# Optimization experiments

Hardware: AMD Instinct MI355X
Metric: run time of the kernel (lower is better)

Reference implementation:

```python
import jax, jax.numpy as jnp
import numpy as np

B, S, H, E = 64, 512, 768, 8
HID = 256

def setup_inputs() -> dict:
    key = jax.random.key(0)
    ks = jax.random.split(key, 20)
    seq = jax.random.normal(ks[0], (B, S, H), dtype=jnp.float32)
    starts = jax.random.randint(ks[1], (B, E), 0, S - 16)
    spans = jax.random.randint(ks[2], (B, E), 0, 12)
    ends = jnp.minimum(starts + spans, S - 1)
    w = lambda k, shp: (jax.random.normal(k, shp, dtype=jnp.float32) * 0.02)
    return {
        "sequence_output": seq,
        "entity_start_positions": starts,
        "entity_end_positions": ends,
        "mW1": w(ks[3], (3 * H, HID)), "mb1": jnp.zeros((HID,), jnp.float32),
        "mW2": w(ks[4], (HID, 3)),     "mb2": jnp.zeros((3,), jnp.float32),
        "pW1": w(ks[5], (3 * H, HID)), "pb1": jnp.zeros((HID,), jnp.float32),
        "pW2": w(ks[6], (HID, 6)),     "pb2": jnp.zeros((6,), jnp.float32),
        "aW1": w(ks[7], (3 * H, HID)), "ab1": jnp.zeros((HID,), jnp.float32),
        "aW2": w(ks[8], (HID, 12)),    "ab2": jnp.zeros((12,), jnp.float32),
        "iW1": w(ks[9], (3 * H, HID)), "ib1": jnp.zeros((HID,), jnp.float32),
        "iW2": w(ks[10], (HID, 4)),    "ib2": jnp.zeros((4,), jnp.float32),
    }

def _mlp(x, W1, b1, W2, b2):
    return jax.nn.relu(x @ W1 + b1) @ W2 + b2  # dropout is inference no-op

def reference(sequence_output, entity_start_positions, entity_end_positions,
              mW1, mb1, mW2, mb2, pW1, pb1, pW2, pb2,
              aW1, ab1, aW2, ab2, iW1, ib1, iW2, ib2):
    Bs, Ss, Hs = sequence_output.shape
    dt = sequence_output.dtype
    # prefix sums: P[b, t] = sum of tokens [0, t)
    P = jnp.concatenate([jnp.zeros((Bs, 1, Hs), dt), jnp.cumsum(sequence_output, axis=1)], axis=1)  # [B,S+1,H]
    s = entity_start_positions  # [B,E]
    e = entity_end_positions    # [B,E]
    bidx = jnp.arange(Bs)[:, None]
    Ps = P[bidx, s]          # [B,E,H] sum of tokens [0, start)
    Pe1 = P[bidx, e + 1]     # [B,E,H] sum of tokens [0, end+1)
    Ptot = P[:, Ss][:, None, :]  # [B,1,H]
    left_n = s.astype(dt)[..., None]
    span_n = (e - s + 1).astype(dt)[..., None]
    right_cnt = (Ss - (e + 1))
    right_n = right_cnt.astype(dt)[..., None]
    left = jnp.where(s[..., None] > 0, Ps / jnp.maximum(left_n, 1.0), 0.0)
    span = (Pe1 - Ps) / span_n
    right = jnp.where(right_cnt[..., None] > 0, (Ptot - Pe1) / jnp.maximum(right_n, 1.0), 0.0)
    emb = jnp.concatenate([left, span, right], axis=-1).reshape(-1, 3 * Hs)  # [N, 3H]
    main_logits = _mlp(emb, mW1, mb1, mW2, mb2)            # [N,3]
    main_probs = jax.nn.softmax(main_logits, axis=-1)
    pred = jnp.argmax(main_probs, axis=-1)                 # [N]
    lp = jax.nn.sigmoid(_mlp(emb, pW1, pb1, pW2, pb2))     # [N,6]
    la = jax.nn.sigmoid(_mlp(emb, aW1, ab1, aW2, ab2))     # [N,12]
    li = jax.nn.sigmoid(_mlp(emb, iW1, ib1, iW2, ib2))     # [N,4]
    fp = jnp.pad(lp, ((0, 0), (0, 16)))
    fa = jnp.pad(la, ((0, 0), (6, 4)))
    fi = jnp.pad(li, ((0, 0), (18, 0)))
    r = pred[:, None]
    fine = jnp.where(r == 0, fp, jnp.where(r == 1, fa, fi))  # [N,22]
    return main_logits, main_probs, fine
```

## Files before the change

### kernel.cpp

```cpp
#include <hip/hip_runtime.h>

#define HH   768
#define SS   512
#define BB   64
#define NE   512
#define K3   2304
#define HID  256
#define NCH  16
#define CRW  32
#define NCOL 1280

typedef __attribute__((ext_vector_type(4))) float  f32x4;
typedef _Float16 f16;
typedef __attribute__((ext_vector_type(8))) _Float16 f16x8;
typedef __attribute__((ext_vector_type(4))) _Float16 f16x4;

__global__ __launch_bounds__(192) void k_scan(
    const float* __restrict__ seq, const int* __restrict__ starts,
    const int* __restrict__ ends, const float* __restrict__ pW1,
    const float* __restrict__ aW1, const float* __restrict__ iW1,
    const float* __restrict__ mW1,
    float* __restrict__ chunkSum, float* __restrict__ cap,
    f16* __restrict__ wT)
{
  __shared__ float Ls[48 * 65];
  const int bx = blockIdx.x;
  const int t  = threadIdx.x;

  if (bx < BB * NCH) {
    const int b = bx >> 4, c = bx & 15;
    int ev[16];
#pragma unroll
    for (int j = 0; j < 8; j++) {
      ev[j]     = starts[b * 8 + j];
      ev[8 + j] = ends[b * 8 + j] + 1;
    }
    unsigned rowhit = 0;
#pragma unroll
    for (int j = 0; j < 16; j++) {
      const int d = ev[j] - c * CRW;
      if ((unsigned)d < 32u) rowhit |= (1u << d);
    }
    const float* base = seq + ((size_t)(b * SS + c * CRW)) * HH + t * 4;
    f32x4 run = {0.f, 0.f, 0.f, 0.f};
#pragma unroll 8
    for (int r = 0; r < CRW; r++) {
      const int s = c * CRW + r;
      if (rowhit & (1u << r)) {
#pragma unroll
        for (int j = 0; j < 16; j++) {
          if (ev[j] == s)
            *(f32x4*)(cap + ((size_t)(b * 16 + j)) * HH + t * 4) = run;
        }
      }
      f32x4 v = *(const f32x4*)(base + (size_t)r * HH);
      run += v;
    }
    *(f32x4*)(chunkSum + ((size_t)(b * 16 + c)) * HH + t * 4) = run;
  } else {
    const int bi   = bx - BB * NCH;
    const int slot = bi / 192;
    const int r    = bi % 192;
    const int kt = r >> 2, nt = r & 3;
    const int k0 = kt * 48, n0 = nt * 64;
    const float* W = (slot == 0) ? pW1 : ((slot == 1) ? aW1 :
                     ((slot == 2) ? iW1 : mW1));
#pragma unroll
    for (int p = 0; p < 4; p++) {
      const int row = (t >> 4) + p * 12;
      const int col = (t & 15) * 4;
      f32x4 v = *(const f32x4*)(W + (size_t)(k0 + row) * HID + n0 + col);
      Ls[row * 65 + col + 0] = v.x;
      Ls[row * 65 + col + 1] = v.y;
      Ls[row * 65 + col + 2] = v.z;
      Ls[row * 65 + col + 3] = v.w;
    }
    __syncthreads();
    const int n = t / 3, u = t % 3;
    if (slot < 3) {
#pragma unroll
      for (int j = 0; j < 2; j++) {
        const int kb = u * 16 + j * 8;
        f16x8 pk;
#pragma unroll
        for (int i = 0; i < 8; i++) pk[i] = (f16)Ls[(kb + i) * 65 + n];
        *(f16x8*)(wT + (size_t)(slot * 256 + n0 + n) * K3 + k0 + kb) = pk;
      }
    } else {
#pragma unroll
      for (int j = 0; j < 2; j++) {
        const int kb = u * 16 + j * 8;
        f16x8 ph, pl;
#pragma unroll
        for (int i = 0; i < 8; i++) {
          const float x = Ls[(kb + i) * 65 + n];
          const f16 h = (f16)x;
          ph[i] = h;
          pl[i] = (f16)(x - (float)h);
        }
        *(f16x8*)(wT + (size_t)(768  + n0 + n) * K3 + k0 + kb) = ph;
        *(f16x8*)(wT + (size_t)(1024 + n0 + n) * K3 + k0 + kb) = pl;
      }
    }
  }
}

__global__ __launch_bounds__(192) void k_emb(
    const float* __restrict__ chunkSum, const float* __restrict__ cap,
    const int* __restrict__ starts, const int* __restrict__ ends,
    f16* __restrict__ embH)
{
  const int bx = blockIdx.x;
  const int t  = threadIdx.x;
  const int b = bx >> 3, e = bx & 7;
  const int s  = starts[b * 8 + e];
  const int en = ends[b * 8 + e];
  const int cs = s >> 5, ce = (en + 1) >> 5;

  const float* csb = chunkSum + (size_t)(b * 16) * HH + t * 4;
  f32x4 acc = {0.f, 0.f, 0.f, 0.f};
  f32x4 baseS = {0.f, 0.f, 0.f, 0.f}, baseE = {0.f, 0.f, 0.f, 0.f};
#pragma unroll
  for (int c = 0; c < 16; c++) {
    if (c == cs) baseS = acc;
    if (c == ce) baseE = acc;
    acc += *(const f32x4*)(csb + (size_t)c * HH);
  }
  f32x4 capS = *(const f32x4*)(cap + (size_t)(b * 16 + e) * HH + t * 4);
  f32x4 capE = *(const f32x4*)(cap + (size_t)(b * 16 + 8 + e) * HH + t * 4);
  f32x4 Ps = baseS + capS;
  f32x4 Pe = baseE + capE;
  f32x4 Pt = acc;

  f32x4 zero = {0.f, 0.f, 0.f, 0.f};
  f32x4 left = zero;
  if (s > 0) left = Ps * (1.0f / (float)s);
  f32x4 span = (Pe - Ps) * (1.0f / (float)(en - s + 1));
  const int rc = SS - (en + 1);
  f32x4 right = zero;
  if (rc > 0) right = (Pt - Pe) * (1.0f / (float)rc);

  f16* ob = embH + (size_t)bx * K3 + t * 4;
  f16x4 p0, p1, p2;
#pragma unroll
  for (int i = 0; i < 4; i++) {
    p0[i] = (f16)left[i];
    p1[i] = (f16)span[i];
    p2[i] = (f16)right[i];
  }
  *(f16x4*)(ob)        = p0;
  *(f16x4*)(ob + 768)  = p1;
  *(f16x4*)(ob + 1536) = p2;
}

__global__ __launch_bounds__(256) void k_gemm(
    const f16* __restrict__ embH, const f16* __restrict__ wT,
    float* __restrict__ Hall)
{
  __shared__ __align__(16) char smem[55296];
  const int bx0 = blockIdx.x;
  const int bx  = (bx0 & 7) * 40 + (bx0 >> 3);
  const int t  = threadIdx.x;
  const int mt = bx & 15, nt = bx >> 4;
  const int m0 = mt * 32, nG0 = nt * 64;

  const int l = t & 63, w = t >> 6;
  const int w2 = w & 1;
  const int kw = w >> 1;
  const int klane = l >> 4;
  const int lr = l & 15;
  f32x4 acc[2][2] = {};

  const int am = t >> 3, ako = (t & 7) * 8;
  const f16* gA = embH + (size_t)(m0 + am) * K3 + ako;
  const int aoff = am * 72 + ako;
  const int bn0 = t >> 3,        bko0 = (t & 7) * 8;
  const int bn1 = (t + 256) >> 3, bko1 = (t & 7) * 8;
  const f16* gB0 = wT + (size_t)(nG0 + bn0) * K3 + bko0;
  const f16* gB1 = wT + (size_t)(nG0 + bn1) * K3 + bko1;
  const int boff0 = bn0 * 72 + bko0, boff1 = bn1 * 72 + bko1;

  f16x8 pA, pB0, pB1, qA, qB0, qB1;

#define LOADSET(S, KT) { const int kn_ = (KT) * 64;                       \
    S##A  = *(const f16x8*)(gA  + kn_);                                   \
    S##B0 = *(const f16x8*)(gB0 + kn_);                                   \
    S##B1 = *(const f16x8*)(gB1 + kn_); }

#define WRITESET(S, BUF) { f16* An_ = (f16*)(smem + (BUF) * 13824);       \
    f16* Bn_ = An_ + 2304;                                                \
    *(f16x8*)(An_ + aoff)  = S##A;                                        \
    *(f16x8*)(Bn_ + boff0) = S##B0;                                       \
    *(f16x8*)(Bn_ + boff1) = S##B1; }

#define COMPUTE(BUF) { f16* Ac_ = (f16*)(smem + (BUF) * 13824);           \
    f16* Bc_ = Ac_ + 2304;                                                \
    const int koff_ = kw * 32 + klane * 8;                                \
    f16x8 aW[2], bE[2];                                                   \
    _Pragma("unroll")                                                     \
    for (int f = 0; f < 2; f++) {                                         \
      aW[f] = *(const f16x8*)(Bc_ + (w2 * 32 + f * 16 + lr) * 72 + koff_);\
      bE[f] = *(const f16x8*)(Ac_ + (f * 16 + lr) * 72 + koff_);          \
    }                                                                     \
    _Pragma("unroll")                                                     \
    for (int fn = 0; fn < 2; fn++)                                        \
      _Pragma("unroll")                                                   \
      for (int fm = 0; fm < 2; fm++)                                      \
        acc[fn][fm] = __builtin_amdgcn_mfma_f32_16x16x32_f16(             \
            aW[fn], bE[fm], acc[fn][fm], 0, 0, 0); }

  LOADSET(p, 0);
  LOADSET(q, 1);
  WRITESET(p, 0);
  WRITESET(q, 1);
  __syncthreads();

  for (int kt = 0; kt < 36; kt += 2) {
    const bool pre = (kt < 34);
    if (pre) { LOADSET(p, kt + 2); LOADSET(q, kt + 3); }
    COMPUTE(kt & 3);
    COMPUTE((kt + 1) & 3);
    if (pre) { WRITESET(p, (kt + 2) & 3); WRITESET(q, (kt + 3) & 3); }
    __syncthreads();
  }
#undef LOADSET
#undef WRITESET
#undef COMPUTE

  float* Lt = (float*)smem;
  if (kw == 1) {
#pragma unroll
    for (int fn = 0; fn < 2; fn++)
#pragma unroll
      for (int fm = 0; fm < 2; fm++) {
        const int nl = w2 * 32 + fn * 16 + klane * 4;
        const int ml = fm * 16 + lr;
        *(f32x4*)(Lt + ml * 68 + nl) = acc[fn][fm];
      }
  }
  __syncthreads();
  if (kw == 0) {
#pragma unroll
    for (int fn = 0; fn < 2; fn++)
#pragma unroll
      for (int fm = 0; fm < 2; fm++) {
        const int nl = w2 * 32 + fn * 16 + klane * 4;
        const int ml = fm * 16 + lr;
        f32x4* pd = (f32x4*)(Lt + ml * 68 + nl);
        *pd = *pd + acc[fn][fm];
      }
  }
  __syncthreads();
  const int row = t >> 3, cb = (t & 7) * 8;
  float* dst = Hall + (size_t)(m0 + row) * NCOL + nG0 + cb;
  const float* src = Lt + row * 68 + cb;
  *(f32x4*)(dst)     = *(const f32x4*)(src);
  *(f32x4*)(dst + 4) = *(const f32x4*)(src + 4);
}

__global__ __launch_bounds__(256) void k_head(
    const float* __restrict__ Hall,
    const float* __restrict__ mb1, const float* __restrict__ mW2, const float* __restrict__ mb2,
    const float* __restrict__ pb1, const float* __restrict__ pW2, const float* __restrict__ pb2,
    const float* __restrict__ ab1, const float* __restrict__ aW2, const float* __restrict__ ab2,
    const float* __restrict__ ib1, const float* __restrict__ iW2, const float* __restrict__ ib2,
    float* __restrict__ out)
{
  __shared__ float red[4][15];
  const int m = blockIdx.x;
  const int t = threadIdx.x;
  const int l = t & 63, wi = t >> 6;
  const int n = t;
  const float* hrow = Hall + (size_t)m * NCOL;

  float h = hrow[768 + n] + hrow[1024 + n] + mb1[n];
  h = h > 0.f ? h : 0.f;
  float am0 = h * mW2[n * 3 + 0];
  float am1 = h * mW2[n * 3 + 1];
  float am2 = h * mW2[n * 3 + 2];

  float hp = hrow[n] + pb1[n];
  hp = hp > 0.f ? hp : 0.f;
  float ha = hrow[256 + n] + ab1[n];
  ha = ha > 0.f ? ha : 0.f;
  float hv = hrow[512 + n] + ib1[n];
  hv = hv > 0.f ? hv : 0.f;

#pragma unroll
  for (int d = 1; d < 64; d <<= 1) {
    am0 += __shfl_xor(am0, d);
    am1 += __shfl_xor(am1, d);
    am2 += __shfl_xor(am2, d);
  }
  if (l == 0) { red[wi][0] = am0; red[wi][1] = am1; red[wi][2] = am2; }
  __syncthreads();

  const float l0 = red[0][0] + red[1][0] + red[2][0] + red[3][0] + mb2[0];
  const float l1 = red[0][1] + red[1][1] + red[2][1] + red[3][1] + mb2[1];
  const float l2 = red[0][2] + red[1][2] + red[2][2] + red[3][2] + mb2[2];
  int pred = 0;
  {
    float pbv = l0;
    if (l1 > pbv) { pbv = l1; pred = 1; }
    if (l2 > pbv) { pbv = l2; pred = 2; }
  }

  if (pred == 0) {
    float ap[6];
#pragma unroll
    for (int o = 0; o < 6; o++) ap[o] = hp * pW2[n * 6 + o];
#pragma unroll
    for (int d = 1; d < 64; d <<= 1)
#pragma unroll
      for (int o = 0; o < 6; o++) ap[o] += __shfl_xor(ap[o], d);
    if (l == 0)
#pragma unroll
      for (int o = 0; o < 6; o++) red[wi][3 + o] = ap[o];
  } else if (pred == 1) {
    float aa[12];
#pragma unroll
    for (int o = 0; o < 12; o++) aa[o] = ha * aW2[n * 12 + o];
#pragma unroll
    for (int d = 1; d < 64; d <<= 1)
#pragma unroll
      for (int o = 0; o < 12; o++) aa[o] += __shfl_xor(aa[o], d);
    if (l == 0)
#pragma unroll
      for (int o = 0; o < 12; o++) red[wi][3 + o] = aa[o];
  } else {
    float ai[4];
#pragma unroll
    for (int o = 0; o < 4; o++) ai[o] = hv * iW2[n * 4 + o];
#pragma unroll
    for (int d = 1; d < 64; d <<= 1)
#pragma unroll
      for (int o = 0; o < 4; o++) ai[o] += __shfl_xor(ai[o], d);
    if (l == 0)
#pragma unroll
      for (int o = 0; o < 4; o++) red[wi][3 + o] = ai[o];
  }
  __syncthreads();

  if (t == 0) {
    const float mx = fmaxf(l0, fmaxf(l1, l2));
    const float e0 = expf(l0 - mx), e1 = expf(l1 - mx), e2 = expf(l2 - mx);
    const float inv = 1.0f / (e0 + e1 + e2);
    const float p0 = e0 * inv, p1 = e1 * inv, p2 = e2 * inv;

    out[m * 3 + 0] = l0;
    out[m * 3 + 1] = l1;
    out[m * 3 + 2] = l2;
    out[1536 + m * 3 + 0] = p0;
    out[1536 + m * 3 + 1] = p1;
    out[1536 + m * 3 + 2] = p2;

    float f[22];
#pragma unroll
    for (int j = 0; j < 22; j++) f[j] = 0.f;
    if (pred == 0) {
#pragma unroll
      for (int j = 0; j < 6; j++) {
        const float v = red[0][3 + j] + red[1][3 + j] + red[2][3 + j] + red[3][3 + j];
        f[j] = 1.0f / (1.0f + expf(-(v + pb2[j])));
      }
    } else if (pred == 1) {
#pragma unroll
      for (int j = 0; j < 12; j++) {
        const float v = red[0][3 + j] + red[1][3 + j] + red[2][3 + j] + red[3][3 + j];
        f[6 + j] = 1.0f / (1.0f + expf(-(v + ab2[j])));
      }
    } else {
#pragma unroll
      for (int j = 0; j < 4; j++) {
        const float v = red[0][3 + j] + red[1][3 + j] + red[2][3 + j] + red[3][3 + j];
        f[18 + j] = 1.0f / (1.0f + expf(-(v + ib2[j])));
      }
    }
#pragma unroll
    for (int j = 0; j < 22; j++) out[3072 + m * 22 + j] = f[j];
  }
}

extern "C" void kernel_launch(void* const* d_in, const int* in_sizes, int n_in,
                              void* d_out, int out_size, void* d_ws, size_t ws_size,
                              hipStream_t stream)
{
  const float* seq    = (const float*)d_in[0];
  const int*   starts = (const int*)d_in[1];
  const int*   ends   = (const int*)d_in[2];
  const float* mW1 = (const float*)d_in[3];
  const float* mb1 = (const float*)d_in[4];
  const float* mW2 = (const float*)d_in[5];
  const float* mb2 = (const float*)d_in[6];
  const float* pW1 = (const float*)d_in[7];
  const float* pb1 = (const float*)d_in[8];
  const float* pW2 = (const float*)d_in[9];
  const float* pb2 = (const float*)d_in[10];
  const float* aW1 = (const float*)d_in[11];
  const float* ab1 = (const float*)d_in[12];
  const float* aW2 = (const float*)d_in[13];
  const float* ab2 = (const float*)d_in[14];
  const float* iW1 = (const float*)d_in[15];
  const float* ib1 = (const float*)d_in[16];
  const float* iW2 = (const float*)d_in[17];
  const float* ib2 = (const float*)d_in[18];

  char* ws = (char*)d_ws;
  float* chunkSum = (float*)(ws);
  float* cap      = (float*)(ws + 3145728);
  f16*   embH     = (f16*)(ws + 6291456);
  f16*   wT       = (f16*)(ws + 8650752);
  float* Hall     = (float*)(ws + 14548992);

  k_scan<<<dim3(1792), dim3(192), 0, stream>>>(seq, starts, ends, pW1, aW1, iW1, mW1,
                                               chunkSum, cap, wT);
  k_emb<<<dim3(512), dim3(192), 0, stream>>>(chunkSum, cap, starts, ends, embH);
  k_gemm<<<dim3(320), dim3(256), 0, stream>>>(embH, wT, Hall);
  k_head<<<dim3(512), dim3(256), 0, stream>>>(Hall,
                                              mb1, mW2, mb2, pb1, pW2, pb2,
                                              ab1, aW2, ab2, ib1, iW2, ib2,
                                              (float*)d_out);
}
```

Before: 50.36 us.

## Load GEMM weight fragments directly from global into registers, bypassing LDS

The GEMM kernel now reads each wave's B (weight) MFMA fragments straight from global memory into registers instead of staging them through shared memory. Only the A (embedding) tile is still staged through LDS, now double-buffered with two barriers per k-step pair. This shrinks LDS from about 54KB to 9KB, which may allow more resident blocks. In exchange, the global reads for B are less coalesced (each lane reads 16 bytes from a different row), and the extra barrier per iteration adds synchronization.

```diff
diff --git a/kernel.cpp b/kernel.cpp
--- a/kernel.cpp
+++ b/kernel.cpp
@@ -157,7 +157,7 @@
     const f16* __restrict__ embH, const f16* __restrict__ wT,
     float* __restrict__ Hall)
 {
-  __shared__ __align__(16) char smem[55296];
+  __shared__ __align__(16) char smem[9216];
   const int bx0 = blockIdx.x;
   const int bx  = (bx0 & 7) * 40 + (bx0 >> 3);
   const int t  = threadIdx.x;
@@ -174,57 +174,48 @@
   const int am = t >> 3, ako = (t & 7) * 8;
   const f16* gA = embH + (size_t)(m0 + am) * K3 + ako;
   const int aoff = am * 72 + ako;
-  const int bn0 = t >> 3,        bko0 = (t & 7) * 8;
-  const int bn1 = (t + 256) >> 3, bko1 = (t & 7) * 8;
-  const f16* gB0 = wT + (size_t)(nG0 + bn0) * K3 + bko0;
-  const f16* gB1 = wT + (size_t)(nG0 + bn1) * K3 + bko1;
-  const int boff0 = bn0 * 72 + bko0, boff1 = bn1 * 72 + bko1;
-
-  f16x8 pA, pB0, pB1, qA, qB0, qB1;
-
-#define LOADSET(S, KT) { const int kn_ = (KT) * 64;                       \
-    S##A  = *(const f16x8*)(gA  + kn_);                                   \
-    S##B0 = *(const f16x8*)(gB0 + kn_);                                   \
-    S##B1 = *(const f16x8*)(gB1 + kn_); }
-
-#define WRITESET(S, BUF) { f16* An_ = (f16*)(smem + (BUF) * 13824);       \
-    f16* Bn_ = An_ + 2304;                                                \
-    *(f16x8*)(An_ + aoff)  = S##A;                                        \
-    *(f16x8*)(Bn_ + boff0) = S##B0;                                       \
-    *(f16x8*)(Bn_ + boff1) = S##B1; }
-
-#define COMPUTE(BUF) { f16* Ac_ = (f16*)(smem + (BUF) * 13824);           \
-    f16* Bc_ = Ac_ + 2304;                                                \
-    const int koff_ = kw * 32 + klane * 8;                                \
-    f16x8 aW[2], bE[2];                                                   \
-    _Pragma("unroll")                                                     \
-    for (int f = 0; f < 2; f++) {                                         \
-      aW[f] = *(const f16x8*)(Bc_ + (w2 * 32 + f * 16 + lr) * 72 + koff_);\
-      bE[f] = *(const f16x8*)(Ac_ + (f * 16 + lr) * 72 + koff_);          \
-    }                                                                     \
-    _Pragma("unroll")                                                     \
-    for (int fn = 0; fn < 2; fn++)                                        \
-      _Pragma("unroll")                                                   \
-      for (int fm = 0; fm < 2; fm++)                                      \
-        acc[fn][fm] = __builtin_amdgcn_mfma_f32_16x16x32_f16(             \
-            aW[fn], bE[fm], acc[fn][fm], 0, 0, 0); }
-
-  LOADSET(p, 0);
-  LOADSET(q, 1);
-  WRITESET(p, 0);
-  WRITESET(q, 1);
+  const f16* gBf0 = wT + (size_t)(nG0 + w2 * 32 + lr) * K3 + kw * 32 + klane * 8;
+  const f16* gBf1 = wT + (size_t)(nG0 + w2 * 32 + 16 + lr) * K3 + kw * 32 + klane * 8;
+
+  f16x8 pA, qA;
+  f16x8 eB0, eB1, oB0, oB1;
+
+#define LOADA(S, KT) { S##A = *(const f16x8*)(gA + (KT) * 64); }
+#define LOADB(S, KT) { S##B0 = *(const f16x8*)(gBf0 + (size_t)(KT) * 64);  \
+                       S##B1 = *(const f16x8*)(gBf1 + (size_t)(KT) * 64); }
+#define WRITEA(S, BUF) { *(f16x8*)((f16*)(smem + (BUF) * 4608) + aoff) = S##A; }
+#define COMPUTE(BUF, S) { f16* Ac_ = (f16*)(smem + (BUF) * 4608);          \
+    const int koff_ = kw * 32 + klane * 8;                                 \
+    f16x8 bE0 = *(const f16x8*)(Ac_ + lr * 72 + koff_);                    \
+    f16x8 bE1 = *(const f16x8*)(Ac_ + (16 + lr) * 72 + koff_);             \
+    acc[0][0] = __builtin_amdgcn_mfma_f32_16x16x32_f16(S##B0, bE0, acc[0][0], 0, 0, 0); \
+    acc[0][1] = __builtin_amdgcn_mfma_f32_16x16x32_f16(S##B0, bE1, acc[0][1], 0, 0, 0); \
+    acc[1][0] = __builtin_amdgcn_mfma_f32_16x16x32_f16(S##B1, bE0, acc[1][0], 0, 0, 0); \
+    acc[1][1] = __builtin_amdgcn_mfma_f32_16x16x32_f16(S##B1, bE1, acc[1][1], 0, 0, 0); }
+
+  LOADA(p, 0);
+  LOADA(q, 1);
+  LOADB(e, 0);
+  LOADB(o, 1);
+  WRITEA(p, 0);
   __syncthreads();
 
   for (int kt = 0; kt < 36; kt += 2) {
     const bool pre = (kt < 34);
-    if (pre) { LOADSET(p, kt + 2); LOADSET(q, kt + 3); }
-    COMPUTE(kt & 3);
-    COMPUTE((kt + 1) & 3);
-    if (pre) { WRITESET(p, (kt + 2) & 3); WRITESET(q, (kt + 3) & 3); }
+    if (pre) LOADA(p, kt + 2);
+    COMPUTE(0, e);
+    if (pre) LOADB(e, kt + 2);
+    WRITEA(q, 1);
     __syncthreads();
-  }
-#undef LOADSET
-#undef WRITESET
+    if (pre) LOADA(q, kt + 3);
+    COMPUTE(1, o);
+    if (pre) LOADB(o, kt + 3);
+    if (pre) WRITEA(p, 0);
+    __syncthreads();
+  }
+#undef LOADA
+#undef LOADB
+#undef WRITEA
 #undef COMPUTE
 
   float* Lt = (float*)smem;
```

After: 56.72 us. 12.6% more time.
